# Performance work log

Measured on AMD Instinct MI355X. Metric: run time of the kernel, lower is better.

The kernel has to match this reference:

```python
import jax, jax.numpy as jnp
import numpy as np

NUM_EMBEDDINGS = 4096
EMBEDDING_DIM = 256
COMMITMENT_COST = 0.25
EPS = 1e-10


def setup_inputs() -> dict:
    key = jax.random.key(0)
    k1, k2 = jax.random.split(key)
    x = jax.random.normal(k1, (32, EMBEDDING_DIM, 32, 32), dtype=jnp.float32)
    # nn.Embedding weight init: uniform(-1/K, 1/K)
    lim = 1.0 / NUM_EMBEDDINGS
    weight = jax.random.uniform(k2, (NUM_EMBEDDINGS, EMBEDDING_DIM),
                                dtype=jnp.float32, minval=-lim, maxval=lim)
    return {"x": x, "weight": weight}


def reference(x, weight):
    B, D, H, W = x.shape
    K = weight.shape[0]
    # [B,D,H,W] -> [B,H,W,D] -> [N,D]
    flat = jnp.transpose(x, (0, 2, 3, 1)).reshape(-1, D)
    distances = (jnp.sum(flat * flat, axis=1, keepdims=True)
                 + jnp.sum(weight * weight, axis=1)
                 - 2.0 * jnp.matmul(flat, weight.T))  # [N,K]
    idx = jnp.argmin(distances, axis=1)  # [N]
    # direct gather == one_hot @ weight (same math, no NxK one-hot materialized)
    quantized = weight[idx].reshape(B, H, W, D)
    quantized = jnp.transpose(quantized, (0, 3, 1, 2))  # [B,D,H,W]
    quantized_st = x + jax.lax.stop_gradient(quantized - x)
    e_latent_loss = jnp.mean((jax.lax.stop_gradient(quantized) - x) ** 2)
    q_latent_loss = jnp.mean((quantized - jax.lax.stop_gradient(x)) ** 2)
    loss = q_latent_loss + COMMITMENT_COST * e_latent_loss
    # avg_probs = mean over tokens of one-hot encodings == normalized histogram
    counts = jnp.zeros((K,), dtype=flat.dtype).at[idx].add(1.0)
    avg_probs = counts / flat.shape[0]
    perplexity = jnp.exp(-jnp.sum(avg_probs * jnp.log(avg_probs + EPS)))
    encoding_indices = idx.reshape(B, H, W)
    return (quantized_st, loss, perplexity, encoding_indices)
```

## Files before the change

### kernel.cpp

```cpp
#include <hip/hip_runtime.h>
#include <math.h>
#include <stdint.h>

#define DIM 256
#define NUME 4096
#define NTOK 32768
#define NELEM 8388608
#define LOSS_OFF 8388608
#define PERP_OFF 8388609
#define IDX_OFF  8388610
#define MARGIN   4.0e-4f
#define ATHR_PAD 1.0e-4f

using short8 = __attribute__((ext_vector_type(8))) short;
using f32x4  = __attribute__((ext_vector_type(4))) float;

__device__ __forceinline__ uint16_t f2bf(float f) {
    uint32_t u = __float_as_uint(f);
    u += 0x7FFFu + ((u >> 16) & 1u);
    return (uint16_t)(u >> 16);
}
__device__ __forceinline__ void gload_lds16(const void* g, void* l) {
    __builtin_amdgcn_global_load_lds(
        (const __attribute__((address_space(1))) void*)g,
        (__attribute__((address_space(3))) void*)l, 16, 0, 0);
}

__global__ void vq_prep(const float* __restrict__ w, uint16_t* __restrict__ wb) {
    int gid = blockIdx.x * 256 + threadIdx.x;
    const float4* src = (const float4*)(w + (size_t)gid * 8);
    float4 a = src[0], c = src[1];
    uint4 o;
    o.x = (uint32_t)f2bf(a.x) | ((uint32_t)f2bf(a.y) << 16);
    o.y = (uint32_t)f2bf(a.z) | ((uint32_t)f2bf(a.w) << 16);
    o.z = (uint32_t)f2bf(c.x) | ((uint32_t)f2bf(c.y) << 16);
    o.w = (uint32_t)f2bf(c.z) | ((uint32_t)f2bf(c.w) << 16);
    *(uint4*)(wb + (size_t)gid * 8) = o;
}

__global__ __launch_bounds__(256, 2)
void vq_mfma(const float* __restrict__ x, const float* __restrict__ wt,
             const uint16_t* __restrict__ wb, float* __restrict__ out,
             int* __restrict__ counts, float* __restrict__ partials) {
    __shared__ __align__(16) char UB[65536];
    __shared__ float sxp[4][64];
    __shared__ float sxS[64];
    __shared__ unsigned gmU[64];
    __shared__ unsigned candCnt[64];
    __shared__ unsigned candL[64 * 16];
    __shared__ int wIdxS[64];
    __shared__ float lred[4];

    const int t    = threadIdx.x;
    const int lane = t & 63;
    const int wv   = t >> 6;
    const int wr   = wv >> 1, wc = wv & 1;
    const int lx   = lane & 15, q = lane >> 4;
    const int wg   = blockIdx.x;
    const int n0   = wg << 6;
    const int b    = n0 >> 10;
    const int p0   = n0 & 1023;
    const float* xbase = x + (size_t)b * (DIM * 1024) + p0;

    if (t < 64) { gmU[t] = 0x7F7FFFFFu; candCnt[t] = 0; }

    {
        int tok = t & 63, w8 = t >> 6;
        const float* p = xbase + (size_t)(w8 * 64) * 1024 + tok;
        float s = 0.f;
        #pragma unroll
        for (int d = 0; d < 64; ++d) s = fmaf(p[(size_t)d * 1024], p[(size_t)d * 1024], s);
        sxp[w8][tok] = s;
    }
    __syncthreads();
    if (t < 64) sxS[t] = (sxp[0][t] + sxp[1][t]) + (sxp[2][t] + sxp[3][t]);

    {
        int dg = t >> 2, c = t & 3;
        #pragma unroll
        for (int it = 0; it < 4; ++it) {
            int d = it * 64 + dg;
            const float* row = xbase + (size_t)d * 1024 + c * 16;
            #pragma unroll
            for (int j = 0; j < 4; ++j) {
                float4 v = *(const float4*)(row + 4 * j);
                float vv[4] = {v.x, v.y, v.z, v.w};
                #pragma unroll
                for (int e = 0; e < 4; ++e) {
                    int tok = c * 16 + 4 * j + e;
                    int byte = (tok << 9) + (d << 1);
                    byte ^= ((tok & 7) << 4);
                    *(uint16_t*)(UB + byte) = f2bf(vv[e]);
                }
            }
        }
    }
    __syncthreads();

    short8 aF[2][8];
    #pragma unroll
    for (int rf = 0; rf < 2; ++rf)
        #pragma unroll
        for (int ks = 0; ks < 8; ++ks) {
            int row = wr * 32 + rf * 16 + lx;
            int byte = (row << 9) + (q << 4) + (ks << 6);
            byte ^= ((row & 7) << 4);
            aF[rf][ks] = *(const short8*)(UB + byte);
        }
    __syncthreads();

    auto STAGE = [&](int k0, int half) {
        #pragma unroll
        for (int i = 0; i < 8; ++i) {
            int o16 = i * 256 + t;
            int code = o16 >> 5, u = o16 & 31;
            const char* src = (const char*)wb + ((size_t)(k0 + code) << 9)
                              + ((u ^ (code & 7)) << 4);
            gload_lds16(src, UB + (half << 15) + (o16 << 4));
        }
    };
    auto COMPUTE = [&](int half, f32x4 acc[2][2]) {
        #pragma unroll
        for (int ks = 0; ks < 8; ++ks) {
            short8 bF[2];
            #pragma unroll
            for (int cf = 0; cf < 2; ++cf) {
                int cr = wc * 32 + cf * 16 + lx;
                int byte = (half << 15) + (cr << 9) + (q << 4) + (ks << 6);
                byte ^= ((cr & 7) << 4);
                bF[cf] = *(const short8*)(UB + byte);
            }
            #pragma unroll
            for (int rf = 0; rf < 2; ++rf)
                #pragma unroll
                for (int cf = 0; cf < 2; ++cf)
                    acc[rf][cf] = __builtin_amdgcn_mfma_f32_16x16x32_bf16(
                        aF[rf][ks], bF[cf], acc[rf][cf], 0, 0, 0);
        }
    };

    float run[2][4];
    #pragma unroll
    for (int rf = 0; rf < 2; ++rf)
        #pragma unroll
        for (int r = 0; r < 4; ++r) run[rf][r] = -3.0e38f;

    STAGE(0, 0);
    for (int tile = 0; tile < 64; ++tile) {
        __syncthreads();
        if (tile < 63) STAGE((tile + 1) * 64, (tile + 1) & 1);
        f32x4 acc[2][2] = {{{0.f,0.f,0.f,0.f},{0.f,0.f,0.f,0.f}},
                           {{0.f,0.f,0.f,0.f},{0.f,0.f,0.f,0.f}}};
        COMPUTE(tile & 1, acc);
        #pragma unroll
        for (int rf = 0; rf < 2; ++rf)
            #pragma unroll
            for (int r = 0; r < 4; ++r)
                run[rf][r] = fmaxf(run[rf][r], fmaxf(acc[rf][0][r], acc[rf][1][r]));
    }
    #pragma unroll
    for (int rf = 0; rf < 2; ++rf)
        #pragma unroll
        for (int r = 0; r < 4; ++r) {
            float m = run[rf][r];
            #pragma unroll
            for (int sh = 1; sh < 16; sh <<= 1) m = fmaxf(m, __shfl_xor(m, sh, 64));
            if (lx == 0) {
                int row = wr * 32 + rf * 16 + q * 4 + r;
                float s = sxS[row] - 2.0f * m;
                atomicMin(&gmU[row], __float_as_uint(s));
            }
        }
    __syncthreads();

    float athr[2][4];
    #pragma unroll
    for (int rf = 0; rf < 2; ++rf)
        #pragma unroll
        for (int r = 0; r < 4; ++r) {
            int row = wr * 32 + rf * 16 + q * 4 + r;
            athr[rf][r] = 0.5f * (sxS[row] - (__uint_as_float(gmU[row]) + MARGIN)) - ATHR_PAD;
        }

    STAGE(0, 0);
    for (int tile = 0; tile < 64; ++tile) {
        __syncthreads();
        if (tile < 63) STAGE((tile + 1) * 64, (tile + 1) & 1);
        f32x4 acc[2][2] = {{{0.f,0.f,0.f,0.f},{0.f,0.f,0.f,0.f}},
                           {{0.f,0.f,0.f,0.f},{0.f,0.f,0.f,0.f}}};
        COMPUTE(tile & 1, acc);
        #pragma unroll
        for (int rf = 0; rf < 2; ++rf)
            #pragma unroll
            for (int r = 0; r < 4; ++r) {
                float a0 = acc[rf][0][r], a1 = acc[rf][1][r];
                if (fmaxf(a0, a1) >= athr[rf][r]) {
                    int row = wr * 32 + rf * 16 + q * 4 + r;
                    int kb = tile * 64 + wc * 32 + lx;
                    if (a0 >= athr[rf][r]) {
                        unsigned s = atomicAdd(&candCnt[row], 1u);
                        if (s < 16) candL[row * 16 + s] = (unsigned)kb;
                    }
                    if (a1 >= athr[rf][r]) {
                        unsigned s = atomicAdd(&candCnt[row], 1u);
                        if (s < 16) candL[row * 16 + s] = (unsigned)(kb + 16);
                    }
                }
            }
    }

    float sqAcc = 0.f;
    for (int ch = 0; ch < 2; ++ch) {
        __syncthreads();
        {
            int dg = t >> 2, c = t & 3;
            #pragma unroll
            for (int it = 0; it < 4; ++it) {
                int d = it * 64 + dg;
                const float* row = xbase + (size_t)d * 1024 + ch * 32 + c * 8;
                float4 f0 = *(const float4*)(row);
                float4 f1 = *(const float4*)(row + 4);
                float vv[8] = {f0.x, f0.y, f0.z, f0.w, f1.x, f1.y, f1.z, f1.w};
                #pragma unroll
                for (int j = 0; j < 8; ++j) {
                    int tl = c * 8 + j;
                    *(float*)(UB + ((tl * 258 + d) << 2)) = vv[j];
                }
            }
        }
        __syncthreads();
        for (int tl = wv; tl < 32; tl += 4) {
            int tok = ch * 32 + tl;
            int nc = candCnt[tok]; if (nc > 16) nc = 16;
            float bs = 3.0e38f; int bi = 0;
            for (int ci = 0; ci < nc; ++ci) {
                int code = (int)candL[tok * 16 + ci];
                float4 wv4 = *(const float4*)(wt + (size_t)code * 256 + lane * 4);
                const float* xr = (const float*)(UB + ((tl * 258 + lane * 4) << 2));
                float p = wv4.x * xr[0];
                p = fmaf(wv4.y, xr[1], p);
                p = fmaf(wv4.z, xr[2], p);
                p = fmaf(wv4.w, xr[3], p);
                #pragma unroll
                for (int sh = 1; sh < 64; sh <<= 1) p += __shfl_xor(p, sh, 64);
                float s = sxS[tok] - 2.0f * p;
                if (s < bs || (s == bs && code < bi)) { bs = s; bi = code; }
            }
            if (lane == 0) wIdxS[tok] = bi;
        }
        __syncthreads();
        {
            int tl = t & 31, db = (t >> 5) * 32;
            int idx = wIdxS[ch * 32 + tl];
            const float* wrow = wt + (size_t)idx * 256;
            float* op = out + (size_t)b * (DIM * 1024) + p0 + ch * 32 + tl;
            #pragma unroll
            for (int j = 0; j < 8; ++j) {
                int d = db + 4 * j;
                float4 q4 = *(const float4*)(wrow + d);
                const float* xr = (const float*)(UB + ((tl * 258 + d) << 2));
                float d0 = q4.x - xr[0], d1 = q4.y - xr[1];
                float d2 = q4.z - xr[2], d3 = q4.w - xr[3];
                sqAcc = fmaf(d0, d0, sqAcc); sqAcc = fmaf(d1, d1, sqAcc);
                sqAcc = fmaf(d2, d2, sqAcc); sqAcc = fmaf(d3, d3, sqAcc);
                op[(size_t)(d + 0) * 1024] = q4.x;
                op[(size_t)(d + 1) * 1024] = q4.y;
                op[(size_t)(d + 2) * 1024] = q4.z;
                op[(size_t)(d + 3) * 1024] = q4.w;
            }
        }
        if (t < 32) {
            int tok = ch * 32 + t;
            out[IDX_OFF + n0 + tok] = (float)wIdxS[tok];
            atomicAdd(&counts[wIdxS[tok]], 1);
        }
    }
    float sq = sqAcc;
    #pragma unroll
    for (int m = 32; m > 0; m >>= 1) sq += __shfl_down(sq, m, 64);
    if (lane == 0) lred[wv] = sq;
    __syncthreads();
    if (t == 0) partials[wg] = (lred[0] + lred[1]) + (lred[2] + lred[3]);
}

#define TM 64
#define TN 64
#define DK 32
#define WS_PAD 68
__global__ __launch_bounds__(256, 2)
void vq_main_fb(const float* __restrict__ x, const float* __restrict__ wt,
                float* __restrict__ out, int* __restrict__ counts,
                float* __restrict__ partials) {
    __shared__ float As[DIM][TM];
    __shared__ float Ws[DK][WS_PAD];
    __shared__ float minv[TM];
    __shared__ int   mini[TM];
    __shared__ float sxp[4][TM];
    __shared__ float sxv[TM];
    __shared__ float lred[4];
    const int t = threadIdx.x, wg = blockIdx.x;
    const int n0 = wg * TM, b = n0 >> 10, p0 = n0 & 1023;
    const float* xb = x + (size_t)b * DIM * 1024 + p0;
    #pragma unroll
    for (int i = 0; i < 16; ++i) {
        int c = t + 256 * i, d = c >> 4, pg = (c & 15) << 2;
        *reinterpret_cast<float4*>(&As[d][pg]) =
            *reinterpret_cast<const float4*>(xb + (size_t)d * 1024 + pg);
    }
    if (t < TM) { minv[t] = 3.0e38f; mini[t] = 0; }
    __syncthreads();
    {
        int tok = t & 63, w = t >> 6;
        float p = 0.0f;
        #pragma unroll
        for (int d = 0; d < 64; ++d) { float v = As[w * 64 + d][tok]; p = fmaf(v, v, p); }
        sxp[w][tok] = p;
    }
    __syncthreads();
    if (t < TM) sxv[t] = (sxp[0][t] + sxp[1][t]) + (sxp[2][t] + sxp[3][t]);
    const int tx = t & 15, ty = t >> 4;
    for (int k0 = 0; k0 < NUME; k0 += TN) {
        float acc[4][4];
        #pragma unroll
        for (int i = 0; i < 4; ++i)
            #pragma unroll
            for (int j = 0; j < 4; ++j) acc[i][j] = 0.0f;
        for (int d0 = 0; d0 < DIM; d0 += DK) {
            __syncthreads();
            int r = t >> 3, dc = (t & 7) << 2;
            #pragma unroll
            for (int h = 0; h < 2; ++h) {
                float4 v = *reinterpret_cast<const float4*>(
                    wt + (size_t)(k0 + r + 32 * h) * DIM + d0 + dc);
                Ws[dc + 0][r + 32 * h] = v.x; Ws[dc + 1][r + 32 * h] = v.y;
                Ws[dc + 2][r + 32 * h] = v.z; Ws[dc + 3][r + 32 * h] = v.w;
            }
            __syncthreads();
            #pragma unroll
            for (int dd = 0; dd < DK; ++dd) {
                float4 a = *reinterpret_cast<const float4*>(&As[d0 + dd][ty << 2]);
                float4 w = *reinterpret_cast<const float4*>(&Ws[dd][tx << 2]);
                float av[4] = {a.x, a.y, a.z, a.w}, wv[4] = {w.x, w.y, w.z, w.w};
                #pragma unroll
                for (int i = 0; i < 4; ++i)
                    #pragma unroll
                    for (int j = 0; j < 4; ++j) acc[i][j] = fmaf(av[i], wv[j], acc[i][j]);
            }
        }
        #pragma unroll
        for (int i = 0; i < 4; ++i) {
            float sxt = sxv[(ty << 2) + i];
            float bv = 3.0e38f; int bi = 0;
            #pragma unroll
            for (int j = 0; j < 4; ++j) {
                float s = sxt - 2.0f * acc[i][j];
                int gi = k0 + (tx << 2) + j;
                if (s < bv) { bv = s; bi = gi; }
            }
            #pragma unroll
            for (int m = 1; m < 16; m <<= 1) {
                float ov = __shfl_xor(bv, m, 64); int oi = __shfl_xor(bi, m, 64);
                if (ov < bv || (ov == bv && oi < bi)) { bv = ov; bi = oi; }
            }
            if (tx == 0) {
                int pl = (ty << 2) + i;
                if (bv < minv[pl]) { minv[pl] = bv; mini[pl] = bi; }
            }
        }
    }
    __syncthreads();
    const int pg = (t & 15) << 2, db = t >> 4;
    int idx4[4];
    #pragma unroll
    for (int j = 0; j < 4; ++j) idx4[j] = mini[pg + j];
    float* outq = out + (size_t)b * DIM * 1024 + p0;
    float sq = 0.0f;
    #pragma unroll
    for (int i = 0; i < 16; ++i) {
        int d = db + (i << 4);
        float4 qv;
        qv.x = wt[(size_t)idx4[0] * DIM + d]; qv.y = wt[(size_t)idx4[1] * DIM + d];
        qv.z = wt[(size_t)idx4[2] * DIM + d]; qv.w = wt[(size_t)idx4[3] * DIM + d];
        float4 xa = *reinterpret_cast<const float4*>(&As[d][pg]);
        float d0_ = qv.x - xa.x, d1_ = qv.y - xa.y, d2_ = qv.z - xa.z, d3_ = qv.w - xa.w;
        sq = fmaf(d0_, d0_, sq); sq = fmaf(d1_, d1_, sq);
        sq = fmaf(d2_, d2_, sq); sq = fmaf(d3_, d3_, sq);
        *reinterpret_cast<float4*>(outq + (size_t)d * 1024 + pg) = qv;
    }
    const int lane = t & 63, wid = t >> 6;
    #pragma unroll
    for (int m = 32; m > 0; m >>= 1) sq += __shfl_down(sq, m, 64);
    if (lane == 0) lred[wid] = sq;
    __syncthreads();
    if (t == 0) partials[wg] = (lred[0] + lred[1]) + (lred[2] + lred[3]);
    if (t < TM) {
        atomicAdd(&counts[mini[t]], 1);
        out[IDX_OFF + n0 + t] = (float)mini[t];
    }
}

__global__ void vq_final(const int* __restrict__ counts,
                         const float* __restrict__ partials,
                         float* __restrict__ out) {
    __shared__ float red[256];
    int t = threadIdx.x;
    red[t] = partials[t] + partials[t + 256];
    __syncthreads();
    for (int m = 128; m > 0; m >>= 1) {
        if (t < m) red[t] += red[t + m];
        __syncthreads();
    }
    if (t == 0) out[LOSS_OFF] = 1.25f * red[0] / (float)NELEM;
    __syncthreads();
    float e = 0.0f;
    for (int c = t; c < NUME; c += 256) {
        float p = (float)counts[c] * (1.0f / (float)NTOK);
        e += p * logf(p + 1e-10f);
    }
    red[t] = e;
    __syncthreads();
    for (int m = 128; m > 0; m >>= 1) {
        if (t < m) red[t] += red[t + m];
        __syncthreads();
    }
    if (t == 0) out[PERP_OFF] = expf(-red[0]);
}

extern "C" void kernel_launch(void* const* d_in, const int* in_sizes, int n_in,
                              void* d_out, int out_size, void* d_ws, size_t ws_size,
                              hipStream_t stream) {
    const float* x  = (const float*)d_in[0];
    const float* wt = (const float*)d_in[1];
    float* out = (float*)d_out;
    const size_t WB_BYTES = (size_t)NUME * DIM * 2;
    const size_t NEED = WB_BYTES + 16384 + 2048;

    if (ws_size >= NEED) {
        uint16_t* wb  = (uint16_t*)d_ws;
        int* counts   = (int*)((char*)d_ws + WB_BYTES);
        float* partials = (float*)((char*)d_ws + WB_BYTES + 16384);
        hipMemsetAsync((char*)d_ws + WB_BYTES, 0, 16384 + 2048, stream);
        vq_prep<<<512, 256, 0, stream>>>(wt, wb);
        vq_mfma<<<512, 256, 0, stream>>>(x, wt, wb, out, counts, partials);
        vq_final<<<1, 256, 0, stream>>>(counts, partials, out);
    } else {
        int* counts   = (int*)d_ws;
        float* partials = (float*)((char*)d_ws + 16384);
        hipMemsetAsync(d_ws, 0, 16384 + 2048, stream);
        vq_main_fb<<<NTOK / TM, 256, 0, stream>>>(x, wt, out, counts, partials);
        vq_final<<<1, 256, 0, stream>>>(counts, partials, out);
    }
}
```

Before: 206.6 us.

## Fuse two codebook passes into one with running-max candidate threshold

Replaces the two-pass scheme (first pass finds each token's max dot product, second pass collects candidates near it) with a single bf16 MFMA pass that keeps a running per-row max via a 16-lane shuffle and collects candidates above a threshold derived from that running max. This removes a full second sweep over the codebook, including the MFMA work and LDS staging. In exchange, every tile now pays a shuffle reduction, and early tiles admit more candidates. So the candidate cap grows to 48, and if a token overflows it, the code falls back to an exact fp32 scan of all 4096 codes for that token, which could be expensive.

```diff
diff --git a/kernel.cpp b/kernel.cpp
--- a/kernel.cpp
+++ b/kernel.cpp
@@ -11,6 +11,7 @@
 #define IDX_OFF  8388610
 #define MARGIN   4.0e-4f
 #define ATHR_PAD 1.0e-4f
+#define CAND_CAP 48
 
 using short8 = __attribute__((ext_vector_type(8))) short;
 using f32x4  = __attribute__((ext_vector_type(4))) float;
@@ -45,9 +46,8 @@
     __shared__ __align__(16) char UB[65536];
     __shared__ float sxp[4][64];
     __shared__ float sxS[64];
-    __shared__ unsigned gmU[64];
     __shared__ unsigned candCnt[64];
-    __shared__ unsigned candL[64 * 16];
+    __shared__ unsigned candL[64 * CAND_CAP];
     __shared__ int wIdxS[64];
     __shared__ float lred[4];
 
@@ -62,7 +62,7 @@
     const int p0   = n0 & 1023;
     const float* xbase = x + (size_t)b * (DIM * 1024) + p0;
 
-    if (t < 64) { gmU[t] = 0x7F7FFFFFu; candCnt[t] = 0; }
+    if (t < 64) candCnt[t] = 0;
 
     {
         int tok = t & 63, w8 = t >> 6;
@@ -139,11 +139,11 @@
         }
     };
 
-    float run[2][4];
+    float runMax[2][4];
     #pragma unroll
     for (int rf = 0; rf < 2; ++rf)
         #pragma unroll
-        for (int r = 0; r < 4; ++r) run[rf][r] = -3.0e38f;
+        for (int r = 0; r < 4; ++r) runMax[rf][r] = -3.0e38f;
 
     STAGE(0, 0);
     for (int tile = 0; tile < 64; ++tile) {
@@ -155,55 +155,25 @@
         #pragma unroll
         for (int rf = 0; rf < 2; ++rf)
             #pragma unroll
-            for (int r = 0; r < 4; ++r)
-                run[rf][r] = fmaxf(run[rf][r], fmaxf(acc[rf][0][r], acc[rf][1][r]));
-    }
-    #pragma unroll
-    for (int rf = 0; rf < 2; ++rf)
-        #pragma unroll
-        for (int r = 0; r < 4; ++r) {
-            float m = run[rf][r];
-            #pragma unroll
-            for (int sh = 1; sh < 16; sh <<= 1) m = fmaxf(m, __shfl_xor(m, sh, 64));
-            if (lx == 0) {
-                int row = wr * 32 + rf * 16 + q * 4 + r;
-                float s = sxS[row] - 2.0f * m;
-                atomicMin(&gmU[row], __float_as_uint(s));
-            }
-        }
-    __syncthreads();
-
-    float athr[2][4];
-    #pragma unroll
-    for (int rf = 0; rf < 2; ++rf)
-        #pragma unroll
-        for (int r = 0; r < 4; ++r) {
-            int row = wr * 32 + rf * 16 + q * 4 + r;
-            athr[rf][r] = 0.5f * (sxS[row] - (__uint_as_float(gmU[row]) + MARGIN)) - ATHR_PAD;
-        }
-
-    STAGE(0, 0);
-    for (int tile = 0; tile < 64; ++tile) {
-        __syncthreads();
-        if (tile < 63) STAGE((tile + 1) * 64, (tile + 1) & 1);
-        f32x4 acc[2][2] = {{{0.f,0.f,0.f,0.f},{0.f,0.f,0.f,0.f}},
-                           {{0.f,0.f,0.f,0.f},{0.f,0.f,0.f,0.f}}};
-        COMPUTE(tile & 1, acc);
-        #pragma unroll
-        for (int rf = 0; rf < 2; ++rf)
-            #pragma unroll
             for (int r = 0; r < 4; ++r) {
                 float a0 = acc[rf][0][r], a1 = acc[rf][1][r];
-                if (fmaxf(a0, a1) >= athr[rf][r]) {
+                float tm = fmaxf(a0, a1);
+                #pragma unroll
+                for (int sh = 1; sh < 16; sh <<= 1)
+                    tm = fmaxf(tm, __shfl_xor(tm, sh, 64));
+                float rm = fmaxf(runMax[rf][r], tm);
+                runMax[rf][r] = rm;
+                float mthr = rm - (0.5f * MARGIN) - ATHR_PAD;
+                if (fmaxf(a0, a1) >= mthr) {
                     int row = wr * 32 + rf * 16 + q * 4 + r;
                     int kb = tile * 64 + wc * 32 + lx;
-                    if (a0 >= athr[rf][r]) {
+                    if (a0 >= mthr) {
                         unsigned s = atomicAdd(&candCnt[row], 1u);
-                        if (s < 16) candL[row * 16 + s] = (unsigned)kb;
+                        if (s < CAND_CAP) candL[row * CAND_CAP + s] = (unsigned)kb;
                     }
-                    if (a1 >= athr[rf][r]) {
+                    if (a1 >= mthr) {
                         unsigned s = atomicAdd(&candCnt[row], 1u);
-                        if (s < 16) candL[row * 16 + s] = (unsigned)(kb + 16);
+                        if (s < CAND_CAP) candL[row * CAND_CAP + s] = (unsigned)(kb + 16);
                     }
                 }
             }
@@ -231,10 +201,12 @@
         __syncthreads();
         for (int tl = wv; tl < 32; tl += 4) {
             int tok = ch * 32 + tl;
-            int nc = candCnt[tok]; if (nc > 16) nc = 16;
+            unsigned ncnt = candCnt[tok];
+            bool ovf = ncnt > CAND_CAP;
+            int count = ovf ? NUME : (int)ncnt;
             float bs = 3.0e38f; int bi = 0;
-            for (int ci = 0; ci < nc; ++ci) {
-                int code = (int)candL[tok * 16 + ci];
+            for (int ci = 0; ci < count; ++ci) {
+                int code = ovf ? ci : (int)candL[tok * CAND_CAP + ci];
                 float4 wv4 = *(const float4*)(wt + (size_t)code * 256 + lane * 4);
                 const float* xr = (const float*)(UB + ((tl * 258 + lane * 4) << 2));
                 float p = wv4.x * xr[0];
@@ -340,11 +312,11 @@
             for (int dd = 0; dd < DK; ++dd) {
                 float4 a = *reinterpret_cast<const float4*>(&As[d0 + dd][ty << 2]);
                 float4 w = *reinterpret_cast<const float4*>(&Ws[dd][tx << 2]);
-                float av[4] = {a.x, a.y, a.z, a.w}, wv[4] = {w.x, w.y, w.z, w.w};
+                float av[4] = {a.x, a.y, a.z, a.w}, wv2[4] = {w.x, w.y, w.z, w.w};
                 #pragma unroll
                 for (int i = 0; i < 4; ++i)
                     #pragma unroll
-                    for (int j = 0; j < 4; ++j) acc[i][j] = fmaf(av[i], wv[j], acc[i][j]);
+                    for (int j = 0; j < 4; ++j) acc[i][j] = fmaf(av[i], wv2[j], acc[i][j]);
             }
         }
         #pragma unroll
```

Measured after the change: 322.6 us. 1.56x slower.
